# Kernel optimization log

Measured on AMD Instinct MI355X. Metric: run time of the kernel, lower is better.

Reference implementation:

```python
import jax, jax.numpy as jnp
import numpy as np

B, N_PER, C, KG, KTOP, KNN = 8, 2048, 256, 16, 512, 32
N = B * N_PER
E = N * KG
EPS = 1e-5


def setup_inputs() -> dict:
    key = jax.random.key(0)
    ks = jax.random.split(key, 32)
    s = 0.05
    x = jax.random.normal(ks[0], (N, C), jnp.float32)
    x_origin = jax.random.normal(ks[1], (N, C), jnp.float32)
    xyz = jax.random.uniform(ks[2], (N, 3), jnp.float32)
    # graph: every node is a dst with KG incoming edges from random nodes of the SAME sample
    edge_dst = jnp.repeat(jnp.arange(N, dtype=jnp.int32), KG)
    src_local = jax.random.randint(ks[3], (E,), 0, N_PER, dtype=jnp.int32)
    edge_src = src_local + (edge_dst // N_PER) * N_PER
    # EdgeConv params (theta on x_j - x_i, phi on x_i)
    theta_w = jax.random.normal(ks[4], (C, C), jnp.float32) * s
    theta_b = jax.random.normal(ks[5], (C,), jnp.float32) * s
    phi_w = jax.random.normal(ks[6], (C, C), jnp.float32) * s
    phi_b = jax.random.normal(ks[7], (C,), jnp.float32) * s
    # region_score_mlp: Conv1d(C,64,1)-ReLU-BN(64)-Conv1d(64,32,1)-ReLU-BN(32)-Conv1d(32,1,1)
    w1 = jax.random.normal(ks[8], (64, C), jnp.float32) * s
    b1 = jax.random.normal(ks[9], (64,), jnp.float32) * s
    g1 = 1.0 + 0.1 * jax.random.normal(ks[10], (64,), jnp.float32)
    be1 = 0.1 * jax.random.normal(ks[11], (64,), jnp.float32)
    m1 = 0.1 * jax.random.normal(ks[12], (64,), jnp.float32)
    v1 = jax.random.uniform(ks[13], (64,), jnp.float32, 0.5, 1.5)
    w2 = jax.random.normal(ks[14], (32, 64), jnp.float32) * s
    b2 = jax.random.normal(ks[15], (32,), jnp.float32) * s
    g2 = 1.0 + 0.1 * jax.random.normal(ks[16], (32,), jnp.float32)
    be2 = 0.1 * jax.random.normal(ks[17], (32,), jnp.float32)
    m2 = 0.1 * jax.random.normal(ks[18], (32,), jnp.float32)
    v2 = jax.random.uniform(ks[19], (32,), jnp.float32, 0.5, 1.5)
    w3 = jax.random.normal(ks[20], (1, 32), jnp.float32) * s
    b3 = jax.random.normal(ks[21], (1,), jnp.float32) * s
    return dict(x=x, x_origin=x_origin, xyz=xyz, edge_src=edge_src, edge_dst=edge_dst,
                theta_w=theta_w, theta_b=theta_b, phi_w=phi_w, phi_b=phi_b,
                w1=w1, b1=b1, g1=g1, be1=be1, m1=m1, v1=v1,
                w2=w2, b2=b2, g2=g2, be2=be2, m2=m2, v2=v2, w3=w3, b3=b3)


def _bn(t, g, b, m, v):
    return (t - m) * jax.lax.rsqrt(v + EPS) * g + b


def _forward(x, x_origin, xyz, edge_src, edge_dst,
             theta_w, theta_b, phi_w, phi_b,
             w1, b1, g1, be1, m1, v1, w2, b2, g2, be2, m2, v2, w3, b3):
    # EdgeConv: h_i = max_{j->i}( theta(x_j - x_i) + phi(x_i) ), then residual add
    msg = ((x[edge_src] - x[edge_dst]) @ theta_w.T + theta_b
           + x[edge_dst] @ phi_w.T + phi_b)                      # [E, C]
    h = jax.ops.segment_max(msg, edge_dst, num_segments=N)       # [N, C]
    x1 = h + x                                                   # residual
    # per-node MLP (Conv1d kernel-size 1 == linear), BN in eval mode
    t = _bn(jax.nn.relu(x1 @ w1.T + b1), g1, be1, m1, v1)
    t = _bn(jax.nn.relu(t @ w2.T + b2), g2, be2, m2, v2)
    score = t @ w3.T + b3                                        # [N, 1]
    score_b = score.reshape(B, N_PER)                            # vps_score
    # per-batch top-k (cls=False path: select by raw score, descending)
    topk_vals, topk_idx = jax.lax.top_k(score_b, KTOP)           # [B, KTOP]
    perm = (topk_idx + jnp.arange(B, dtype=topk_idx.dtype)[:, None] * N_PER).reshape(-1)
    x_new = x1[perm].reshape(B, KTOP, C)
    x_copy = x_origin[perm].reshape(B, KTOP, -1)
    xyz_sel = xyz[perm].reshape(B, KTOP, 3)
    # rebuild 32-NN graph per sample on selected points (batched, no per-b python calls)
    d2 = jnp.sum((xyz_sel[:, :, None, :] - xyz_sel[:, None, :, :]) ** 2, axis=-1)  # [B,K,K]
    _, knn_idx = jax.lax.top_k(-d2, KNN)                         # [B, KTOP, 32]
    return knn_idx, x_new, x_copy, score_b, topk_vals


def reference(x, x_origin, xyz, edge_src, edge_dst,
              theta_w, theta_b, phi_w, phi_b,
              w1, b1, g1, be1, m1, v1, w2, b2, g2, be2, m2, v2, w3, b3):
    return _forward(x, x_origin, xyz, edge_src, edge_dst,
                    theta_w, theta_b, phi_w, phi_b,
                    w1, b1, g1, be1, m1, v1, w2, b2, g2, be2, m2, v2, w3, b3)
```

## Files before the change

### kernel.cpp

```cpp
#include <hip/hip_runtime.h>
#include <math.h>

constexpr int B     = 8;
constexpr int N_PER = 2048;
constexpr int C     = 256;
constexpr int KG    = 16;
constexpr int KTOP  = 512;
constexpr int KNN   = 32;
constexpr int N     = B * N_PER;
constexpr float EPS = 1e-5f;

typedef __attribute__((ext_vector_type(8))) short  short8;
typedef __attribute__((ext_vector_type(4))) float  f32x4;

__device__ inline void split3(float f, unsigned short& h, unsigned short& m,
                              unsigned short& l)
{
    const unsigned u  = __float_as_uint(f);
    const unsigned r1 = (u + 0x7FFFu + ((u >> 16) & 1u)) & 0xFFFF0000u;
    h = (unsigned short)(r1 >> 16);
    const float f2 = f - __uint_as_float(r1);
    const unsigned u2 = __float_as_uint(f2);
    const unsigned r2 = (u2 + 0x7FFFu + ((u2 >> 16) & 1u)) & 0xFFFF0000u;
    m = (unsigned short)(r2 >> 16);
    const float f3 = f2 - __uint_as_float(r2);
    const unsigned u3 = __float_as_uint(f3);
    l = (unsigned short)((u3 + 0x7FFFu + ((u3 >> 16) & 1u)) >> 16);
}

__device__ inline void split8v(const float* __restrict__ s,
                               unsigned short* __restrict__ dh,
                               unsigned short* __restrict__ dm,
                               unsigned short* __restrict__ dl)
{
    float4 a = *(const float4*)s;
    float4 b = *(const float4*)(s + 4);
    float v[8] = {a.x, a.y, a.z, a.w, b.x, b.y, b.z, b.w};
    short8 h8, m8, l8;
    unsigned short hh, mm, ll;
#pragma unroll
    for (int j = 0; j < 8; ++j) {
        split3(v[j], hh, mm, ll);
        h8[j] = (short)hh;
        m8[j] = (short)mm;
        l8[j] = (short)ll;
    }
    *(short8*)dh = h8;
    *(short8*)dm = m8;
    *(short8*)dl = l8;
}

constexpr int GX = N * C / 8;
constexpr int GW = C * C / 8;

__global__ __launch_bounds__(256) void k0_split(
    const float* __restrict__ x, const float* __restrict__ thw,
    const float* __restrict__ phw,
    unsigned short* __restrict__ xh, unsigned short* __restrict__ xm,
    unsigned short* __restrict__ xl,
    unsigned short* __restrict__ th, unsigned short* __restrict__ tm,
    unsigned short* __restrict__ tl,
    unsigned short* __restrict__ ph, unsigned short* __restrict__ pm,
    unsigned short* __restrict__ pl)
{
    const int g = blockIdx.x * 256 + threadIdx.x;
    if (g < GX) {
        const int o = g * 8;
        split8v(x + o, xh + o, xm + o, xl + o);
    } else if (g < GX + GW) {
        const int o = (g - GX) * 8;
        split8v(thw + o, th + o, tm + o, tl + o);
    } else if (g < GX + 2 * GW) {
        const int o = (g - GX - GW) * 8;
        split8v(phw + o, ph + o, pm + o, pl + o);
    }
}

__global__ __launch_bounds__(256, 2) void k1_planes(
    const unsigned short* __restrict__ xh, const unsigned short* __restrict__ xm,
    const unsigned short* __restrict__ xl,
    const unsigned short* __restrict__ th, const unsigned short* __restrict__ tm,
    const unsigned short* __restrict__ tl,
    const unsigned short* __restrict__ ph, const unsigned short* __restrict__ pm,
    const unsigned short* __restrict__ pl,
    const float* __restrict__ x, const float* __restrict__ thb,
    const float* __restrict__ phb, float* __restrict__ T, float* __restrict__ R)
{
    const int tid  = threadIdx.x;
    const int row0 = blockIdx.x * 64;
    const int n0   = blockIdx.y * 64;
    const int lane = tid & 63;
    const int wv   = tid >> 6;
    const int wr   = (wv >> 1) * 32;
    const int wc   = (wv & 1) * 32;
    const int fr   = lane & 15;
    const int fk   = (lane >> 4) * 8;

    f32x4 acTh[2][2], acTl[2][2], acQh[2][2], acQl[2][2];
    const f32x4 zz = {0.f, 0.f, 0.f, 0.f};
#pragma unroll
    for (int m = 0; m < 2; ++m)
#pragma unroll
        for (int n = 0; n < 2; ++n) {
            acTh[m][n] = zz; acTl[m][n] = zz;
            acQh[m][n] = zz; acQl[m][n] = zz;
        }

    const size_t aOff = (size_t)(row0 + wr + fr) * C + fk;
    const size_t bOff = (size_t)(n0 + wc + fr) * C + fk;

    for (int k0 = 0; k0 < C; k0 += 32) {
        short8 a1f[2], a2f[2], a3f[2];
#pragma unroll
        for (int m = 0; m < 2; ++m) {
            const size_t o = aOff + (size_t)m * 16 * C + k0;
            a1f[m] = *(const short8*)(xh + o);
            a2f[m] = *(const short8*)(xm + o);
            a3f[m] = *(const short8*)(xl + o);
        }

        {
            short8 b1f[2], b2f[2], b3f[2];
#pragma unroll
            for (int n = 0; n < 2; ++n) {
                const size_t o = bOff + (size_t)n * 16 * C + k0;
                b1f[n] = *(const short8*)(th + o);
                b2f[n] = *(const short8*)(tm + o);
                b3f[n] = *(const short8*)(tl + o);
            }
#pragma unroll
            for (int m = 0; m < 2; ++m)
#pragma unroll
                for (int n = 0; n < 2; ++n) {
                    acTh[m][n] = __builtin_amdgcn_mfma_f32_16x16x32_bf16(a1f[m], b1f[n], acTh[m][n], 0, 0, 0);
                    acTl[m][n] = __builtin_amdgcn_mfma_f32_16x16x32_bf16(a2f[m], b1f[n], acTl[m][n], 0, 0, 0);
                    acTl[m][n] = __builtin_amdgcn_mfma_f32_16x16x32_bf16(a3f[m], b1f[n], acTl[m][n], 0, 0, 0);
                }
#pragma unroll
            for (int m = 0; m < 2; ++m)
#pragma unroll
                for (int n = 0; n < 2; ++n) {
                    acTl[m][n] = __builtin_amdgcn_mfma_f32_16x16x32_bf16(a1f[m], b2f[n], acTl[m][n], 0, 0, 0);
                    acTl[m][n] = __builtin_amdgcn_mfma_f32_16x16x32_bf16(a2f[m], b2f[n], acTl[m][n], 0, 0, 0);
                }
#pragma unroll
            for (int m = 0; m < 2; ++m)
#pragma unroll
                for (int n = 0; n < 2; ++n) {
                    acTl[m][n] = __builtin_amdgcn_mfma_f32_16x16x32_bf16(a1f[m], b3f[n], acTl[m][n], 0, 0, 0);
                }
        }

        {
            short8 b1f[2], b2f[2], b3f[2];
#pragma unroll
            for (int n = 0; n < 2; ++n) {
                const size_t o = bOff + (size_t)n * 16 * C + k0;
                b1f[n] = *(const short8*)(ph + o);
                b2f[n] = *(const short8*)(pm + o);
                b3f[n] = *(const short8*)(pl + o);
            }
#pragma unroll
            for (int m = 0; m < 2; ++m)
#pragma unroll
                for (int n = 0; n < 2; ++n) {
                    acQh[m][n] = __builtin_amdgcn_mfma_f32_16x16x32_bf16(a1f[m], b1f[n], acQh[m][n], 0, 0, 0);
                    acQl[m][n] = __builtin_amdgcn_mfma_f32_16x16x32_bf16(a2f[m], b1f[n], acQl[m][n], 0, 0, 0);
                    acQl[m][n] = __builtin_amdgcn_mfma_f32_16x16x32_bf16(a3f[m], b1f[n], acQl[m][n], 0, 0, 0);
                }
#pragma unroll
            for (int m = 0; m < 2; ++m)
#pragma unroll
                for (int n = 0; n < 2; ++n) {
                    acQl[m][n] = __builtin_amdgcn_mfma_f32_16x16x32_bf16(a1f[m], b2f[n], acQl[m][n], 0, 0, 0);
                    acQl[m][n] = __builtin_amdgcn_mfma_f32_16x16x32_bf16(a2f[m], b2f[n], acQl[m][n], 0, 0, 0);
                }
#pragma unroll
            for (int m = 0; m < 2; ++m)
#pragma unroll
                for (int n = 0; n < 2; ++n) {
                    acQl[m][n] = __builtin_amdgcn_mfma_f32_16x16x32_bf16(a1f[m], b3f[n], acQl[m][n], 0, 0, 0);
                }
        }
    }

    const int cr = (lane >> 4) * 4;
#pragma unroll
    for (int m = 0; m < 2; ++m) {
#pragma unroll
        for (int n = 0; n < 2; ++n) {
            const int col  = n0 + wc + n * 16 + fr;
            const float bias = thb[col] + phb[col];
#pragma unroll
            for (int j = 0; j < 4; ++j) {
                const int row = row0 + wr + m * 16 + cr + j;
                const size_t off = (size_t)row * C + col;
                const float tval = acTh[m][n][j] + acTl[m][n][j];
                const float qval = acQh[m][n][j] + acQl[m][n][j];
                T[off] = tval;
                R[off] = x[off] + qval + bias - tval;
            }
        }
    }
}

__device__ inline void cvt_store24(unsigned short* dh, unsigned short* dm,
                                   unsigned short* dl, float4 a, float4 b)
{
    short8 h, m, l;
    unsigned short hh, mm, ll;
    float v[8] = {a.x, a.y, a.z, a.w, b.x, b.y, b.z, b.w};
#pragma unroll
    for (int j = 0; j < 8; ++j) {
        split3(v[j], hh, mm, ll);
        h[j] = (short)hh;
        m[j] = (short)mm;
        l[j] = (short)ll;
    }
    *(short8*)dh = h;
    *(short8*)dm = m;
    *(short8*)dl = l;
}

__global__ __launch_bounds__(256) void k1_fb(
    const float* __restrict__ x, const float* __restrict__ thw,
    const float* __restrict__ phw, const float* __restrict__ thb,
    const float* __restrict__ phb, float* __restrict__ T, float* __restrict__ R)
{
    constexpr int BM = 128, BN = 64, ST = 40;
    __shared__ unsigned short sA[3][BM * ST];
    __shared__ unsigned short sT[3][BN * ST];
    __shared__ unsigned short sP[3][BN * ST];

    const int tid  = threadIdx.x;
    const int row0 = blockIdx.x * BM;
    const int n0   = blockIdx.y * BN;
    const int lane = tid & 63;
    const int wv   = tid >> 6;
    const int wr   = (wv >> 1) * 64;
    const int wc   = (wv & 1) * 32;
    const int fr   = lane & 15;
    const int fk   = (lane >> 4) * 8;
    const int ar0 = tid >> 2;
    const int ac  = (tid & 3) * 8;

    f32x4 acTh[4][2], acTl[4][2], acQh[4][2], acQl[4][2];
    const f32x4 zz = {0.f, 0.f, 0.f, 0.f};
#pragma unroll
    for (int m = 0; m < 4; ++m)
#pragma unroll
        for (int n = 0; n < 2; ++n) {
            acTh[m][n] = zz; acTl[m][n] = zz;
            acQh[m][n] = zz; acQl[m][n] = zz;
        }

    const float* xA0 = x   + (size_t)(row0 + ar0)      * C + ac;
    const float* xA1 = x   + (size_t)(row0 + 64 + ar0) * C + ac;
    const float* wT  = thw + (size_t)(n0 + ar0)        * C + ac;
    const float* wP  = phw + (size_t)(n0 + ar0)        * C + ac;

    float4 a0a = *(const float4*)(xA0 + 0), a0b = *(const float4*)(xA0 + 4);
    float4 a1a = *(const float4*)(xA1 + 0), a1b = *(const float4*)(xA1 + 4);
    float4 ta  = *(const float4*)(wT  + 0), tb_ = *(const float4*)(wT  + 4);
    float4 pa  = *(const float4*)(wP  + 0), pb_ = *(const float4*)(wP  + 4);

    const int sOffA0 = ar0 * ST + ac;
    const int sOffA1 = (64 + ar0) * ST + ac;
    const int aBase  = (wr + fr) * ST + fk;
    const int bBase  = (wc + fr) * ST + fk;

    for (int step = 0; step < 8; ++step) {
        __syncthreads();
        cvt_store24(sA[0] + sOffA0, sA[1] + sOffA0, sA[2] + sOffA0, a0a, a0b);
        cvt_store24(sA[0] + sOffA1, sA[1] + sOffA1, sA[2] + sOffA1, a1a, a1b);
        cvt_store24(sT[0] + sOffA0, sT[1] + sOffA0, sT[2] + sOffA0, ta,  tb_);
        cvt_store24(sP[0] + sOffA0, sP[1] + sOffA0, sP[2] + sOffA0, pa,  pb_);
        __syncthreads();

        if (step < 7) {
            const int kn = (step + 1) * 32;
            a0a = *(const float4*)(xA0 + kn); a0b = *(const float4*)(xA0 + kn + 4);
            a1a = *(const float4*)(xA1 + kn); a1b = *(const float4*)(xA1 + kn + 4);
            ta  = *(const float4*)(wT  + kn); tb_ = *(const float4*)(wT  + kn + 4);
            pa  = *(const float4*)(wP  + kn); pb_ = *(const float4*)(wP  + kn + 4);
        }

        short8 a1f[4], a2f[4], a3f[4];
#pragma unroll
        for (int m = 0; m < 4; ++m) {
            const int r = aBase + m * 16 * ST;
            a1f[m] = *(const short8*)(sA[0] + r);
            a2f[m] = *(const short8*)(sA[1] + r);
            a3f[m] = *(const short8*)(sA[2] + r);
        }
        {
            short8 t0[2], p0[2];
#pragma unroll
            for (int n = 0; n < 2; ++n) {
                const int r = bBase + n * 16 * ST;
                t0[n] = *(const short8*)(sT[0] + r);
                p0[n] = *(const short8*)(sP[0] + r);
            }
#pragma unroll
            for (int m = 0; m < 4; ++m)
#pragma unroll
                for (int n = 0; n < 2; ++n) {
                    acTh[m][n] = __builtin_amdgcn_mfma_f32_16x16x32_bf16(a1f[m], t0[n], acTh[m][n], 0, 0, 0);
                    acQh[m][n] = __builtin_amdgcn_mfma_f32_16x16x32_bf16(a1f[m], p0[n], acQh[m][n], 0, 0, 0);
                    acTl[m][n] = __builtin_amdgcn_mfma_f32_16x16x32_bf16(a2f[m], t0[n], acTl[m][n], 0, 0, 0);
                    acQl[m][n] = __builtin_amdgcn_mfma_f32_16x16x32_bf16(a2f[m], p0[n], acQl[m][n], 0, 0, 0);
                    acTl[m][n] = __builtin_amdgcn_mfma_f32_16x16x32_bf16(a3f[m], t0[n], acTl[m][n], 0, 0, 0);
                    acQl[m][n] = __builtin_amdgcn_mfma_f32_16x16x32_bf16(a3f[m], p0[n], acQl[m][n], 0, 0, 0);
                }
        }
        {
            short8 t1[2], p1[2];
#pragma unroll
            for (int n = 0; n < 2; ++n) {
                const int r = bBase + n * 16 * ST;
                t1[n] = *(const short8*)(sT[1] + r);
                p1[n] = *(const short8*)(sP[1] + r);
            }
#pragma unroll
            for (int m = 0; m < 4; ++m)
#pragma unroll
                for (int n = 0; n < 2; ++n) {
                    acTl[m][n] = __builtin_amdgcn_mfma_f32_16x16x32_bf16(a1f[m], t1[n], acTl[m][n], 0, 0, 0);
                    acQl[m][n] = __builtin_amdgcn_mfma_f32_16x16x32_bf16(a1f[m], p1[n], acQl[m][n], 0, 0, 0);
                    acTl[m][n] = __builtin_amdgcn_mfma_f32_16x16x32_bf16(a2f[m], t1[n], acTl[m][n], 0, 0, 0);
                    acQl[m][n] = __builtin_amdgcn_mfma_f32_16x16x32_bf16(a2f[m], p1[n], acQl[m][n], 0, 0, 0);
                }
        }
        {
            short8 t2[2], p2[2];
#pragma unroll
            for (int n = 0; n < 2; ++n) {
                const int r = bBase + n * 16 * ST;
                t2[n] = *(const short8*)(sT[2] + r);
                p2[n] = *(const short8*)(sP[2] + r);
            }
#pragma unroll
            for (int m = 0; m < 4; ++m)
#pragma unroll
                for (int n = 0; n < 2; ++n) {
                    acTl[m][n] = __builtin_amdgcn_mfma_f32_16x16x32_bf16(a1f[m], t2[n], acTl[m][n], 0, 0, 0);
                    acQl[m][n] = __builtin_amdgcn_mfma_f32_16x16x32_bf16(a1f[m], p2[n], acQl[m][n], 0, 0, 0);
                }
        }
    }

    const int cr = (lane >> 4) * 4;
#pragma unroll
    for (int m = 0; m < 4; ++m) {
#pragma unroll
        for (int n = 0; n < 2; ++n) {
            const int col  = n0 + wc + n * 16 + fr;
            const float bias = thb[col] + phb[col];
#pragma unroll
            for (int j = 0; j < 4; ++j) {
                const int row = row0 + wr + m * 16 + cr + j;
                const size_t off = (size_t)row * C + col;
                const float tval = acTh[m][n][j] + acTl[m][n][j];
                const float qval = acQh[m][n][j] + acQl[m][n][j];
                T[off] = tval;
                R[off] = x[off] + qval + bias - tval;
            }
        }
    }
}

__global__ __launch_bounds__(256) void k2a_gather_max(
    const int* __restrict__ esrc, const float* __restrict__ T, float* x1r)
{
    const int gb = blockIdx.x;
    const int b  = gb & 7;
    const int node0 = b * N_PER + (gb >> 3) * 4;
    const int t = threadIdx.x;
    __shared__ int s[4][KG];
    if (t < 64) s[t >> 4][t & 15] = esrc[(node0 + (t >> 4)) * KG + (t & 15)];
    __syncthreads();
    const int m  = t >> 6;
    const int c4 = (t & 63) * 4;
    float4 acc = make_float4(-INFINITY, -INFINITY, -INFINITY, -INFINITY);
#pragma unroll
    for (int k = 0; k < KG; ++k) {
        const float4 v = *(const float4*)&T[(size_t)s[m][k] * C + c4];
        acc.x = fmaxf(acc.x, v.x);  acc.y = fmaxf(acc.y, v.y);
        acc.z = fmaxf(acc.z, v.z);  acc.w = fmaxf(acc.w, v.w);
    }
    const size_t off = (size_t)(node0 + m) * C + c4;
    float4 r = *(const float4*)&x1r[off];
    r.x += acc.x;  r.y += acc.y;  r.z += acc.z;  r.w += acc.w;
    *(float4*)&x1r[off] = r;
}

__global__ __launch_bounds__(256) void k2bc_score(
    const float* __restrict__ x1, const float* __restrict__ w1,
    const float* __restrict__ b1, const float* __restrict__ g1,
    const float* __restrict__ be1, const float* __restrict__ m1,
    const float* __restrict__ v1,
    const float* __restrict__ w2, const float* __restrict__ b2,
    const float* __restrict__ g2, const float* __restrict__ be2,
    const float* __restrict__ m2, const float* __restrict__ v2,
    const float* __restrict__ w3, const float* __restrict__ b3,
    float* __restrict__ score_ws, float* __restrict__ out_score)
{
    constexpr int BK = 16, ST = 68;
    __shared__ float Xs[BK * ST];
    __shared__ float Ws[BK * ST];
    __shared__ float t1s[64 * 65];
    __shared__ float w2s[32 * 65];
    __shared__ float w3s[32];
    __shared__ float zs[64 * 33];
    const int tid  = threadIdx.x;
    const int row0 = blockIdx.x * 64;
    const int tx = tid & 15, ty = tid >> 4;
    const int lm = tid >> 2, lq = (tid & 3) << 2;

    float acc[4][4] = {{0.f}};
    for (int k0 = 0; k0 < C; k0 += BK) {
        float4 fx = *(const float4*)(x1 + (size_t)(row0 + lm) * C + k0 + lq);
        float4 fw = *(const float4*)(w1 + (size_t)lm * C + k0 + lq);
        __syncthreads();
        Xs[(lq + 0) * ST + lm] = fx.x;  Xs[(lq + 1) * ST + lm] = fx.y;
        Xs[(lq + 2) * ST + lm] = fx.z;  Xs[(lq + 3) * ST + lm] = fx.w;
        Ws[(lq + 0) * ST + lm] = fw.x;  Ws[(lq + 1) * ST + lm] = fw.y;
        Ws[(lq + 2) * ST + lm] = fw.z;  Ws[(lq + 3) * ST + lm] = fw.w;
        __syncthreads();
#pragma unroll
        for (int k = 0; k < BK; ++k) {
            float4 a4 = *(const float4*)&Xs[k * ST + (ty << 2)];
            float4 w4 = *(const float4*)&Ws[k * ST + (tx << 2)];
            float av[4] = {a4.x, a4.y, a4.z, a4.w};
            float wv[4] = {w4.x, w4.y, w4.z, w4.w};
#pragma unroll
            for (int i2 = 0; i2 < 4; ++i2)
#pragma unroll
                for (int j2 = 0; j2 < 4; ++j2) acc[i2][j2] += av[i2] * wv[j2];
        }
    }
    __syncthreads();
#pragma unroll
    for (int i2 = 0; i2 < 4; ++i2) {
        const int mrow = (ty << 2) + i2;
#pragma unroll
        for (int j2 = 0; j2 < 4; ++j2) {
            const int o = (tx << 2) + j2;
            float y = acc[i2][j2] + b1[o];
            y = fmaxf(y, 0.f);
            y = (y - m1[o]) * (1.0f / sqrtf(v1[o] + EPS)) * g1[o] + be1[o];
            t1s[mrow * 65 + o] = y;
        }
    }
    for (int idx = tid; idx < 2048; idx += 256)
        w2s[(idx >> 6) * 65 + (idx & 63)] = w2[idx];
    if (tid < 32) w3s[tid] = w3[tid];
    __syncthreads();

    const int o = tid & 31;
    const float inv2 = (1.0f / sqrtf(v2[o] + EPS)) * g2[o];
#pragma unroll
    for (int p = 0; p < 8; ++p) {
        const int nl = p * 8 + (tid >> 5);
        float z = 0.f;
#pragma unroll
        for (int j = 0; j < 64; ++j) z += t1s[nl * 65 + j] * w2s[o * 65 + j];
        z += b2[o];
        z = fmaxf(z, 0.f);
        z = (z - m2[o]) * inv2 + be2[o];
        zs[nl * 33 + o] = z;
    }
    __syncthreads();

    if (tid < 64) {
        float sacc = 0.f;
#pragma unroll
        for (int j = 0; j < 32; ++j) sacc += zs[tid * 33 + j] * w3s[j];
        sacc += b3[0];
        const int node = row0 + tid;
        score_ws[node]  = sacc;
        out_score[node] = sacc;
    }
}

__global__ __launch_bounds__(1024) void k3_topk(
    const float* __restrict__ score, const float* __restrict__ xyz,
    float* __restrict__ out_topk, int* __restrict__ perm,
    float* __restrict__ xsel)
{
    __shared__ unsigned long long keys[N_PER];
    const int b = blockIdx.x;
    const int t = threadIdx.x;
    for (int i = t; i < N_PER; i += 1024) {
        const float v = score[b * N_PER + i];
        unsigned u = __float_as_uint(v);
        const unsigned ua = (u & 0x80000000u) ? ~u : (u | 0x80000000u);
        const unsigned ud = ~ua;
        keys[i] = ((unsigned long long)ud << 32) | (unsigned)i;
    }
    __syncthreads();
    for (int k = 2; k <= N_PER; k <<= 1) {
        for (int j = k >> 1; j > 0; j >>= 1) {
            for (int i = t; i < N_PER; i += 1024) {
                const int ixj = i ^ j;
                if (ixj > i) {
                    const unsigned long long a = keys[i], c = keys[ixj];
                    const bool up = ((i & k) == 0);
                    if ((a > c) == up) { keys[i] = c; keys[ixj] = a; }
                }
            }
            __syncthreads();
        }
    }
    for (int r = t; r < KTOP; r += 1024) {
        const int idx = (int)(keys[r] & 0xffffffffu);
        const int g = b * N_PER + idx;
        out_topk[b * KTOP + r] = score[g];
        perm[b * KTOP + r] = g;
        xsel[(b * KTOP + r) * 3 + 0] = xyz[g * 3 + 0];
        xsel[(b * KTOP + r) * 3 + 1] = xyz[g * 3 + 1];
        xsel[(b * KTOP + r) * 3 + 2] = xyz[g * 3 + 2];
    }
}

__global__ __launch_bounds__(256) void k5_knn(
    const int* __restrict__ perm, const float* __restrict__ xsel,
    const float* __restrict__ x1, const float* __restrict__ xorig,
    float* __restrict__ out_xnew, float* __restrict__ out_xcopy,
    float* __restrict__ out_knn)
{
    constexpr int G = 4;
    __shared__ float px[KTOP], py[KTOP], pz[KTOP];
    __shared__ unsigned long long keys[G * KTOP];
    const int t  = threadIdx.x;
    const int q0 = blockIdx.x * G;
    const int b  = q0 >> 9;
    const int i0 = q0 & 511;

    for (int idx = t; idx < KTOP; idx += 256) {
        const size_t base = ((size_t)b * KTOP + idx) * 3;
        px[idx] = xsel[base + 0];
        py[idx] = xsel[base + 1];
        pz[idx] = xsel[base + 2];
    }
#pragma unroll
    for (int p = 0; p < G; ++p) {
        const int row = q0 + p;
        const int g = perm[row];
        out_xnew [(size_t)row * C + t] = x1   [(size_t)g * C + t];
        out_xcopy[(size_t)row * C + t] = xorig[(size_t)g * C + t];
    }
    __syncthreads();

    for (int w = t; w < G * KTOP; w += 256) {
        const int p = w >> 9, idx = w & 511;
        const float dx = __fsub_rn(px[i0 + p], px[idx]);
        const float dy = __fsub_rn(py[i0 + p], py[idx]);
        const float dz = __fsub_rn(pz[i0 + p], pz[idx]);
        const float d2 = __fadd_rn(__fadd_rn(__fmul_rn(dx, dx), __fmul_rn(dy, dy)),
                                   __fmul_rn(dz, dz));
        keys[w] = ((unsigned long long)__float_as_uint(d2) << 32) | (unsigned)idx;
    }
    __syncthreads();

    for (int k = 2; k <= 32; k <<= 1) {
        for (int j = k >> 1; j > 0; j >>= 1) {
            for (int i = t; i < G * KTOP; i += 256) {
                const int ixj = i ^ j;
                if (ixj > i) {
                    const int il = i & 31;
                    const unsigned long long a = keys[i], c = keys[ixj];
                    const bool up = ((il & k) == 0) || (k == 32);
                    if ((a > c) == up) { keys[i] = c; keys[ixj] = a; }
                }
            }
            __syncthreads();
        }
    }
    for (int r = 0; r < 4; ++r) {
        const int npairs = 8 >> r;
        const int total  = G * npairs * 32;
        for (int w = t; w < total; w += 256) {
            const int p  = w / (npairs * 32);
            const int rm = w - p * (npairs * 32);
            const int m  = rm >> 5, i = rm & 31;
            const int baseA = p * KTOP + m * (64 << r);
            const int baseB = baseA + (32 << r);
            const unsigned long long a = keys[baseA + i];
            const unsigned long long c = keys[baseB + 31 - i];
            keys[baseA + i] = (c < a) ? c : a;
        }
        __syncthreads();
        for (int j = 16; j > 0; j >>= 1) {
            for (int w = t; w < total; w += 256) {
                const int p  = w / (npairs * 32);
                const int rm = w - p * (npairs * 32);
                const int m  = rm >> 5, i = rm & 31;
                const int ixj = i ^ j;
                if (ixj > i) {
                    const int baseA = p * KTOP + m * (64 << r);
                    const unsigned long long a = keys[baseA + i], c = keys[baseA + ixj];
                    if (a > c) { keys[baseA + i] = c; keys[baseA + ixj] = a; }
                }
            }
            __syncthreads();
        }
    }

    if (t < G * KNN) {
        const int p = t >> 5, r = t & 31;
        out_knn[((size_t)(q0 + p)) * KNN + r] =
            (float)(unsigned)(keys[p * KTOP + r] & 0xffffffffu);
    }
}

extern "C" void kernel_launch(void* const* d_in, const int* in_sizes, int n_in,
                              void* d_out, int out_size, void* d_ws, size_t ws_size,
                              hipStream_t stream)
{
    const float* x     = (const float*)d_in[0];
    const float* xorig = (const float*)d_in[1];
    const float* xyz   = (const float*)d_in[2];
    const int*   esrc  = (const int*)d_in[3];
    const float* thw = (const float*)d_in[5];
    const float* thb = (const float*)d_in[6];
    const float* phw = (const float*)d_in[7];
    const float* phb = (const float*)d_in[8];
    const float* w1  = (const float*)d_in[9];
    const float* b1  = (const float*)d_in[10];
    const float* g1  = (const float*)d_in[11];
    const float* be1 = (const float*)d_in[12];
    const float* m1  = (const float*)d_in[13];
    const float* v1  = (const float*)d_in[14];
    const float* w2  = (const float*)d_in[15];
    const float* b2  = (const float*)d_in[16];
    const float* g2  = (const float*)d_in[17];
    const float* be2 = (const float*)d_in[18];
    const float* m2  = (const float*)d_in[19];
    const float* v2  = (const float*)d_in[20];
    const float* w3  = (const float*)d_in[21];
    const float* b3  = (const float*)d_in[22];

    float* ws   = (float*)d_ws;
    float* T    = ws;
    float* x1   = ws + (size_t)N * C;
    float* sc   = ws + 2 * (size_t)N * C;
    int*   perm = (int*)(sc + N);
    float* xsel = (float*)(perm + B * KTOP);

    unsigned short* xh = (unsigned short*)(xsel + (size_t)B * KTOP * 3);
    unsigned short* xm = xh + (size_t)N * C;
    unsigned short* xl = xm + (size_t)N * C;
    unsigned short* th = xl + (size_t)N * C;
    unsigned short* tm = th + (size_t)C * C;
    unsigned short* tl = tm + (size_t)C * C;
    unsigned short* ph = tl + (size_t)C * C;
    unsigned short* pm = ph + (size_t)C * C;
    unsigned short* pl = pm + (size_t)C * C;
    const size_t ws_need = (size_t)((char*)(pl + (size_t)C * C) - (char*)ws);
    const bool planes_ok = (ws_size >= ws_need);

    float* out     = (float*)d_out;
    float* o_knn   = out;
    float* o_xnew  = o_knn + (size_t)B * KTOP * KNN;
    float* o_xcopy = o_xnew + (size_t)B * KTOP * C;
    float* o_score = o_xcopy + (size_t)B * KTOP * C;
    float* o_topk  = o_score + (size_t)B * N_PER;

    if (planes_ok) {
        const int ngroups = GX + 2 * GW;
        k0_split<<<(ngroups + 255) / 256, 256, 0, stream>>>(
            x, thw, phw, xh, xm, xl, th, tm, tl, ph, pm, pl);
        k1_planes<<<dim3(N / 64, C / 64), 256, 0, stream>>>(
            xh, xm, xl, th, tm, tl, ph, pm, pl, x, thb, phb, T, x1);
    } else {
        k1_fb<<<dim3(N / 128, C / 64), 256, 0, stream>>>(x, thw, phw, thb, phb, T, x1);
    }
    k2a_gather_max<<<N / 4, 256, 0, stream>>>(esrc, T, x1);
    k2bc_score<<<N / 64, 256, 0, stream>>>(x1, w1, b1, g1, be1, m1, v1,
                                           w2, b2, g2, be2, m2, v2, w3, b3, sc, o_score);
    k3_topk<<<B, 1024, 0, stream>>>(sc, xyz, o_topk, perm, xsel);
    k5_knn<<<B * KTOP / 4, 256, 0, stream>>>(perm, xsel, x1, xorig,
                                             o_xnew, o_xcopy, o_knn);
}
```

Measured before the change: 294.2 us.

## Stage split-bf16 GEMM operands in LDS with 128x64 tiles and register prefetch

The split-precision dual GEMM (theta and phi) now stages the three bf16 planes of x and both weight sets in shared memory, using a padded stride to avoid bank conflicts. Before, each wave loaded its fragments straight from global memory. The block tile grows to 128x64, so each wave computes a 64x32 region and reuses its A fragments across both weight matrices. The next k-slice is prefetched into registers while the current slice's MFMAs run. The cost is larger accumulator register pressure (32 f32x4 accumulators) and dropping the 2-blocks-per-CU launch bound, which may lower occupancy.

```diff
diff --git a/kernel.cpp b/kernel.cpp
--- a/kernel.cpp
+++ b/kernel.cpp
@@ -76,7 +76,7 @@
     }
 }
 
-__global__ __launch_bounds__(256, 2) void k1_planes(
+__global__ __launch_bounds__(256) void k1_hyb(
     const unsigned short* __restrict__ xh, const unsigned short* __restrict__ xm,
     const unsigned short* __restrict__ xl,
     const unsigned short* __restrict__ th, const unsigned short* __restrict__ tm,
@@ -86,107 +86,154 @@
     const float* __restrict__ x, const float* __restrict__ thb,
     const float* __restrict__ phb, float* __restrict__ T, float* __restrict__ R)
 {
+    constexpr int BM = 128, BN = 64, ST = 40;
+    __shared__ unsigned short sA[3][BM * ST];
+    __shared__ unsigned short sT[3][BN * ST];
+    __shared__ unsigned short sP[3][BN * ST];
+
     const int tid  = threadIdx.x;
-    const int row0 = blockIdx.x * 64;
-    const int n0   = blockIdx.y * 64;
+    const int row0 = blockIdx.x * BM;
+    const int n0   = blockIdx.y * BN;
     const int lane = tid & 63;
     const int wv   = tid >> 6;
-    const int wr   = (wv >> 1) * 32;
+    const int wr   = (wv >> 1) * 64;
     const int wc   = (wv & 1) * 32;
     const int fr   = lane & 15;
     const int fk   = (lane >> 4) * 8;
-
-    f32x4 acTh[2][2], acTl[2][2], acQh[2][2], acQl[2][2];
+    const int ar0  = tid >> 2;
+    const int ac   = (tid & 3) * 8;
+
+    f32x4 acTh[4][2], acTl[4][2], acQh[4][2], acQl[4][2];
     const f32x4 zz = {0.f, 0.f, 0.f, 0.f};
 #pragma unroll
-    for (int m = 0; m < 2; ++m)
+    for (int m = 0; m < 4; ++m)
 #pragma unroll
         for (int n = 0; n < 2; ++n) {
             acTh[m][n] = zz; acTl[m][n] = zz;
             acQh[m][n] = zz; acQl[m][n] = zz;
         }
 
-    const size_t aOff = (size_t)(row0 + wr + fr) * C + fk;
-    const size_t bOff = (size_t)(n0 + wc + fr) * C + fk;
-
-    for (int k0 = 0; k0 < C; k0 += 32) {
-        short8 a1f[2], a2f[2], a3f[2];
-#pragma unroll
-        for (int m = 0; m < 2; ++m) {
-            const size_t o = aOff + (size_t)m * 16 * C + k0;
-            a1f[m] = *(const short8*)(xh + o);
-            a2f[m] = *(const short8*)(xm + o);
-            a3f[m] = *(const short8*)(xl + o);
-        }
-
+    const size_t offA0 = (size_t)(row0 + ar0)      * C + ac;
+    const size_t offA1 = (size_t)(row0 + 64 + ar0) * C + ac;
+    const size_t offW  = (size_t)(n0 + ar0)        * C + ac;
+
+    short8 rA0h = *(const short8*)(xh + offA0);
+    short8 rA0m = *(const short8*)(xm + offA0);
+    short8 rA0l = *(const short8*)(xl + offA0);
+    short8 rA1h = *(const short8*)(xh + offA1);
+    short8 rA1m = *(const short8*)(xm + offA1);
+    short8 rA1l = *(const short8*)(xl + offA1);
+    short8 rTh  = *(const short8*)(th + offW);
+    short8 rTm  = *(const short8*)(tm + offW);
+    short8 rTl  = *(const short8*)(tl + offW);
+    short8 rPh  = *(const short8*)(ph + offW);
+    short8 rPm  = *(const short8*)(pm + offW);
+    short8 rPl  = *(const short8*)(pl + offW);
+
+    const int sOffA0 = ar0 * ST + ac;
+    const int sOffA1 = (64 + ar0) * ST + ac;
+    const int aBase  = (wr + fr) * ST + fk;
+    const int bBase  = (wc + fr) * ST + fk;
+
+    for (int step = 0; step < 8; ++step) {
+        __syncthreads();
+        *(short8*)(sA[0] + sOffA0) = rA0h;
+        *(short8*)(sA[1] + sOffA0) = rA0m;
+        *(short8*)(sA[2] + sOffA0) = rA0l;
+        *(short8*)(sA[0] + sOffA1) = rA1h;
+        *(short8*)(sA[1] + sOffA1) = rA1m;
+        *(short8*)(sA[2] + sOffA1) = rA1l;
+        *(short8*)(sT[0] + sOffA0) = rTh;
+        *(short8*)(sT[1] + sOffA0) = rTm;
+        *(short8*)(sT[2] + sOffA0) = rTl;
+        *(short8*)(sP[0] + sOffA0) = rPh;
+        *(short8*)(sP[1] + sOffA0) = rPm;
+        *(short8*)(sP[2] + sOffA0) = rPl;
+        __syncthreads();
+
+        if (step < 7) {
+            const int kn = (step + 1) * 32;
+            rA0h = *(const short8*)(xh + offA0 + kn);
+            rA0m = *(const short8*)(xm + offA0 + kn);
+            rA0l = *(const short8*)(xl + offA0 + kn);
+            rA1h = *(const short8*)(xh + offA1 + kn);
+            rA1m = *(const short8*)(xm + offA1 + kn);
+            rA1l = *(const short8*)(xl + offA1 + kn);
+            rTh  = *(const short8*)(th + offW + kn);
+            rTm  = *(const short8*)(tm + offW + kn);
+            rTl  = *(const short8*)(tl + offW + kn);
+            rPh  = *(const short8*)(ph + offW + kn);
+            rPm  = *(const short8*)(pm + offW + kn);
+            rPl  = *(const short8*)(pl + offW + kn);
+        }
+
+        short8 a1f[4], a2f[4], a3f[4];
+#pragma unroll
+        for (int m = 0; m < 4; ++m) {
+            const int r = aBase + m * 16 * ST;
+            a1f[m] = *(const short8*)(sA[0] + r);
+            a2f[m] = *(const short8*)(sA[1] + r);
+            a3f[m] = *(const short8*)(sA[2] + r);
+        }
         {
-            short8 b1f[2], b2f[2], b3f[2];
+            short8 t0[2], p0[2];
 #pragma unroll
             for (int n = 0; n < 2; ++n) {
-                const size_t o = bOff + (size_t)n * 16 * C + k0;
-                b1f[n] = *(const short8*)(th + o);
-                b2f[n] = *(const short8*)(tm + o);
-                b3f[n] = *(const short8*)(tl + o);
-            }
-#pragma unroll
-            for (int m = 0; m < 2; ++m)
+                const int r = bBase + n * 16 * ST;
+                t0[n] = *(const short8*)(sT[0] + r);
+                p0[n] = *(const short8*)(sP[0] + r);
+            }
+#pragma unroll
+            for (int m = 0; m < 4; ++m)
 #pragma unroll
                 for (int n = 0; n < 2; ++n) {
-                    acTh[m][n] = __builtin_amdgcn_mfma_f32_16x16x32_bf16(a1f[m], b1f[n], acTh[m][n], 0, 0, 0);
-                    acTl[m][n] = __builtin_amdgcn_mfma_f32_16x16x32_bf16(a2f[m], b1f[n], acTl[m][n], 0, 0, 0);
-                    acTl[m][n] = __builtin_amdgcn_mfma_f32_16x16x32_bf16(a3f[m], b1f[n], acTl[m][n], 0, 0, 0);
-                }
-#pragma unroll
-            for (int m = 0; m < 2; ++m)
+                    acTh[m][n] = __builtin_amdgcn_mfma_f32_16x16x32_bf16(a1f[m], t0[n], acTh[m][n], 0, 0, 0);
+                    acQh[m][n] = __builtin_amdgcn_mfma_f32_16x16x32_bf16(a1f[m], p0[n], acQh[m][n], 0, 0, 0);
+                    acTl[m][n] = __builtin_amdgcn_mfma_f32_16x16x32_bf16(a2f[m], t0[n], acTl[m][n], 0, 0, 0);
+                    acQl[m][n] = __builtin_amdgcn_mfma_f32_16x16x32_bf16(a2f[m], p0[n], acQl[m][n], 0, 0, 0);
+                    acTl[m][n] = __builtin_amdgcn_mfma_f32_16x16x32_bf16(a3f[m], t0[n], acTl[m][n], 0, 0, 0);
+                    acQl[m][n] = __builtin_amdgcn_mfma_f32_16x16x32_bf16(a3f[m], p0[n], acQl[m][n], 0, 0, 0);
+                }
+        }
+        {
+            short8 t1[2], p1[2];
+#pragma unroll
+            for (int n = 0; n < 2; ++n) {
+                const int r = bBase + n * 16 * ST;
+                t1[n] = *(const short8*)(sT[1] + r);
+                p1[n] = *(const short8*)(sP[1] + r);
+            }
+#pragma unroll
+            for (int m = 0; m < 4; ++m)
 #pragma unroll
                 for (int n = 0; n < 2; ++n) {
-                    acTl[m][n] = __builtin_amdgcn_mfma_f32_16x16x32_bf16(a1f[m], b2f[n], acTl[m][n], 0, 0, 0);
-                    acTl[m][n] = __builtin_amdgcn_mfma_f32_16x16x32_bf16(a2f[m], b2f[n], acTl[m][n], 0, 0, 0);
-                }
-#pragma unroll
-            for (int m = 0; m < 2; ++m)
+                    acTl[m][n] = __builtin_amdgcn_mfma_f32_16x16x32_bf16(a1f[m], t1[n], acTl[m][n], 0, 0, 0);
+                    acQl[m][n] = __builtin_amdgcn_mfma_f32_16x16x32_bf16(a1f[m], p1[n], acQl[m][n], 0, 0, 0);
+                    acTl[m][n] = __builtin_amdgcn_mfma_f32_16x16x32_bf16(a2f[m], t1[n], acTl[m][n], 0, 0, 0);
+                    acQl[m][n] = __builtin_amdgcn_mfma_f32_16x16x32_bf16(a2f[m], p1[n], acQl[m][n], 0, 0, 0);
+                }
+        }
+        {
+            short8 t2[2], p2[2];
+#pragma unroll
+            for (int n = 0; n < 2; ++n) {
+                const int r = bBase + n * 16 * ST;
+                t2[n] = *(const short8*)(sT[2] + r);
+                p2[n] = *(const short8*)(sP[2] + r);
+            }
+#pragma unroll
+            for (int m = 0; m < 4; ++m)
 #pragma unroll
                 for (int n = 0; n < 2; ++n) {
-                    acTl[m][n] = __builtin_amdgcn_mfma_f32_16x16x32_bf16(a1f[m], b3f[n], acTl[m][n], 0, 0, 0);
-                }
-        }
-
-        {
-            short8 b1f[2], b2f[2], b3f[2];
-#pragma unroll
-            for (int n = 0; n < 2; ++n) {
-                const size_t o = bOff + (size_t)n * 16 * C + k0;
-                b1f[n] = *(const short8*)(ph + o);
-                b2f[n] = *(const short8*)(pm + o);
-                b3f[n] = *(const short8*)(pl + o);
-            }
-#pragma unroll
-            for (int m = 0; m < 2; ++m)
-#pragma unroll
-                for (int n = 0; n < 2; ++n) {
-                    acQh[m][n] = __builtin_amdgcn_mfma_f32_16x16x32_bf16(a1f[m], b1f[n], acQh[m][n], 0, 0, 0);
-                    acQl[m][n] = __builtin_amdgcn_mfma_f32_16x16x32_bf16(a2f[m], b1f[n], acQl[m][n], 0, 0, 0);
-                    acQl[m][n] = __builtin_amdgcn_mfma_f32_16x16x32_bf16(a3f[m], b1f[n], acQl[m][n], 0, 0, 0);
-                }
-#pragma unroll
-            for (int m = 0; m < 2; ++m)
-#pragma unroll
-                for (int n = 0; n < 2; ++n) {
-                    acQl[m][n] = __builtin_amdgcn_mfma_f32_16x16x32_bf16(a1f[m], b2f[n], acQl[m][n], 0, 0, 0);
-                    acQl[m][n] = __builtin_amdgcn_mfma_f32_16x16x32_bf16(a2f[m], b2f[n], acQl[m][n], 0, 0, 0);
-                }
-#pragma unroll
-            for (int m = 0; m < 2; ++m)
-#pragma unroll
-                for (int n = 0; n < 2; ++n) {
-                    acQl[m][n] = __builtin_amdgcn_mfma_f32_16x16x32_bf16(a1f[m], b3f[n], acQl[m][n], 0, 0, 0);
+                    acTl[m][n] = __builtin_amdgcn_mfma_f32_16x16x32_bf16(a1f[m], t2[n], acTl[m][n], 0, 0, 0);
+                    acQl[m][n] = __builtin_amdgcn_mfma_f32_16x16x32_bf16(a1f[m], p2[n], acQl[m][n], 0, 0, 0);
                 }
         }
     }
 
     const int cr = (lane >> 4) * 4;
 #pragma unroll
-    for (int m = 0; m < 2; ++m) {
+    for (int m = 0; m < 4; ++m) {
 #pragma unroll
         for (int n = 0; n < 2; ++n) {
             const int col  = n0 + wc + n * 16 + fr;
@@ -671,7 +718,7 @@
         const int ngroups = GX + 2 * GW;
         k0_split<<<(ngroups + 255) / 256, 256, 0, stream>>>(
             x, thw, phw, xh, xm, xl, th, tm, tl, ph, pm, pl);
-        k1_planes<<<dim3(N / 64, C / 64), 256, 0, stream>>>(
+        k1_hyb<<<dim3(N / 128, C / 64), 256, 0, stream>>>(
             xh, xm, xl, th, tm, tl, ph, pm, pl, x, thb, phb, T, x1);
     } else {
         k1_fb<<<dim3(N / 128, C / 64), 256, 0, stream>>>(x, thw, phw, thb, phb, T, x1);
```

After: 271.9 us. 1.08x faster.
